# Kernel optimization log

Hardware: AMD Instinct MI355X
Metric: run time of the kernel (lower is better)

## Reference

```python
import jax, jax.numpy as jnp
import numpy as np

B, N, K = 16, 8192, 16
H1, H3 = 512, 64
EPS = 1e-5


def _bn(x, g, b):
    # BatchNorm1d training-mode math: normalize per-channel (last axis) over all other axes.
    ax = tuple(range(x.ndim - 1))
    m = x.mean(ax, keepdims=True)
    v = x.var(ax, keepdims=True)  # biased variance, as in torch BN forward
    return (x - m) * jax.lax.rsqrt(v + EPS) * g + b


def _gather(h, idx):
    # h: [b,n,f], idx: [b,n,k] -> [b,n,k,f] per-batch neighbor gather
    return jax.vmap(lambda hb, ib: hb[ib])(h, idx)


def _forward(data, knn, e1_w, e1_b, e1_g, e1_be,
             gc1_w, gc1_b, g1_g, g1_be, gc2_w, gc2_b, g2_g, g2_be,
             e2_w, e2_b, e2_g, e2_be,
             d1_w, d1_b, d1_g, d1_be, d2_w, d2_b, d2_g, d2_be):
    b, n, _ = data.shape
    # local covariance features
    neigh = _gather(data, knn)                       # [b,n,K,3]
    cen = neigh - neigh.mean(axis=2, keepdims=True)
    cov = jnp.einsum('bnki,bnkj->bnij', cen, cen) / (K - 1)
    x = jnp.concatenate([data, cov.reshape(b, n, 9)], axis=-1)  # [b,n,12]
    # e_layers1: Linear(12,h3) + BN + ReLU
    x = jax.nn.relu(_bn(x @ e1_w + e1_b, e1_g, e1_be))
    # GCNConv over uniform-degree kNN graph with self loop: (h_i + sum_j h_j)/(K+1)
    deg = float(K + 1)
    h = x @ gc1_w
    h = (h + _gather(h, knn).sum(axis=2)) / deg + gc1_b
    x = jax.nn.relu(_bn(h, g1_g, g1_be))
    h = x @ gc2_w
    h = (h + _gather(h, knn).sum(axis=2)) / deg + gc2_b
    x = jax.nn.relu(_bn(h, g2_g, g2_be))             # [b,n,h1]
    # AdaptiveMaxPool1d(1) over nodes
    x = x.max(axis=1, keepdims=True)                 # [b,1,h1]
    # e_layers2: Linear(h1,h1) + BN + ReLU
    x = jax.nn.relu(_bn(x @ e2_w + e2_b, e2_g, e2_be))
    # decode: folding grid
    nx_ = int(1 + (n * 120 / 60) ** 0.5)
    ny_ = int(1 + (n * 60 / 120) ** 0.5)
    xg = jnp.linspace(1.0, 120.0, nx_)
    yg = jnp.linspace(1.0, 60.0, ny_)
    grid = jnp.stack(jnp.meshgrid(xg, yg, indexing='ij'), axis=-1).reshape(-1, 2)[:n]
    kfeat = jnp.broadcast_to(x, (b, n, x.shape[-1]))  # codeword repeated per node
    y = jnp.broadcast_to(grid[None], (b, n, 2))
    z = jnp.concatenate([kfeat, y], axis=-1)          # [b,n,h1+2]
    z = jax.nn.relu(_bn(z @ d1_w + d1_b, d1_g, d1_be))
    z = jnp.concatenate([kfeat, z], axis=-1)          # [b,n,h1+3]
    z = jax.nn.relu(_bn(z @ d2_w + d2_b, d2_g, d2_be))
    return z                                          # [b,n,3]


def setup_inputs() -> dict:
    key = jax.random.key(0)
    ks = jax.random.split(key, 8)

    def lin(k, i, o):
        s = 1.0 / np.sqrt(i)
        return jax.random.uniform(k, (i, o), jnp.float32, -s, s)

    ones = lambda c: jnp.ones((c,), jnp.float32)
    zeros = lambda c: jnp.zeros((c,), jnp.float32)
    return {
        'data': jax.random.normal(ks[0], (B, N, 3), jnp.float32),
        'knn': jax.random.randint(ks[1], (B, N, K), 0, N),
        'e1_w': lin(ks[2], 12, H3), 'e1_b': zeros(H3), 'e1_g': ones(H3), 'e1_be': zeros(H3),
        'gc1_w': lin(ks[3], H3, 2 * H3), 'gc1_b': zeros(2 * H3), 'g1_g': ones(2 * H3), 'g1_be': zeros(2 * H3),
        'gc2_w': lin(ks[4], 2 * H3, H1), 'gc2_b': zeros(H1), 'g2_g': ones(H1), 'g2_be': zeros(H1),
        'e2_w': lin(ks[5], H1, H1), 'e2_b': zeros(H1), 'e2_g': ones(H1), 'e2_be': zeros(H1),
        'd1_w': lin(ks[6], H1 + 2, 3), 'd1_b': zeros(3), 'd1_g': ones(3), 'd1_be': zeros(3),
        'd2_w': lin(ks[7], H1 + 3, 3), 'd2_b': zeros(3), 'd2_g': ones(3), 'd2_be': zeros(3),
    }


def reference(data, knn, e1_w, e1_b, e1_g, e1_be,
              gc1_w, gc1_b, g1_g, g1_be, gc2_w, gc2_b, g2_g, g2_be,
              e2_w, e2_b, e2_g, e2_be,
              d1_w, d1_b, d1_g, d1_be, d2_w, d2_b, d2_g, d2_be):
    return _forward(data, knn, e1_w, e1_b, e1_g, e1_be,
                    gc1_w, gc1_b, g1_g, g1_be, gc2_w, gc2_b, g2_g, g2_be,
                    e2_w, e2_b, e2_g, e2_be,
                    d1_w, d1_b, d1_g, d1_be, d2_w, d2_b, d2_g, d2_be)
```

## Files before the change

kernel.cpp:

```cpp
#include <hip/hip_runtime.h>
#include <hip/hip_fp16.h>
#include <stdint.h>

#define BATCH 16
#define NPTS  8192
#define KNN   16
#define NROWS (BATCH*NPTS)
#define EPSBN 1e-5f
#define DEGINV (1.0f/17.0f)

typedef _Float16 f16x8 __attribute__((ext_vector_type(8)));
typedef float    f32x4 __attribute__((ext_vector_type(4)));

__device__ __forceinline__ unsigned short f2hu(float f) {
    union { _Float16 h; unsigned short u; } cv;
    cv.h = (_Float16)f;
    return cv.u;
}
__device__ __forceinline__ float hu2f(unsigned short u) {
    union { unsigned short u; _Float16 h; } cv;
    cv.u = u;
    return (float)cv.h;
}
__device__ __forceinline__ unsigned fenc(float f) {
    unsigned u = __float_as_uint(f);
    return (int)u >= 0 ? (u | 0x80000000u) : ~u;
}
__device__ __forceinline__ float fdec(unsigned k) {
    return (k & 0x80000000u) ? __uint_as_float(k & 0x7FFFFFFFu) : __uint_as_float(~k);
}

#define SZ_S1    0
#define SZ_S2P   128
#define SZ_S3P   16512
#define SZ_S4    82048
#define SZ_C1    83072
#define SZ_GN    83080
#define SZ_D2    83088
#define SZ_SCSH1 83096
#define SZ_SCSH2 83224
#define SZ_TOT   83480

__global__ __launch_bounds__(256) void k_prep(
    const float* __restrict__ gc1w, const float* __restrict__ gc2w,
    const float* __restrict__ d1w, const float* __restrict__ d1b,
    unsigned short* __restrict__ W1T, unsigned short* __restrict__ W2T,
    float* __restrict__ gn, float* __restrict__ statszone, unsigned* __restrict__ mm)
{
    int t = blockIdx.x * 256 + threadIdx.x;
    int NT_ = gridDim.x * 256;
    for (int i = t; i < 65536; i += NT_) {
        int c = i >> 7, k = i & 127;
        W2T[i] = f2hu(gc2w[k * 512 + c]);
    }
    for (int i = t; i < 8192; i += NT_) {
        int c = i >> 6, k = i & 63;
        W1T[i] = f2hu(gc1w[k * 128 + c]);
    }
    for (int i = t; i < SZ_TOT; i += NT_) statszone[i] = 0.f;
    for (int i = t; i < 8192; i += NT_) mm[i] = 0u;
    for (int i = t; i < 8192; i += NT_) mm[8192 + i] = 0xFFFFFFFFu;
    for (int n = t; n < 8192; n += NT_) {
        int ix = n / 65, iy = n % 65;
        float gx = 1.f + ix * (119.f / 128.f);
        float gy = 1.f + iy * (59.f / 64.f);
        #pragma unroll
        for (int j = 0; j < 3; j++)
            gn[n * 3 + j] = gx * d1w[512 * 3 + j] + gy * d1w[513 * 3 + j] + d1b[j];
    }
}

__global__ __launch_bounds__(256) void k_cov_e1(
    const float* __restrict__ data, const int* __restrict__ knn,
    const float* __restrict__ e1w, const float* __restrict__ e1b,
    float* __restrict__ a1)
{
    __shared__ float w[12 * 64];
    __shared__ float bias[64];
    int tid = threadIdx.x;
    for (int i = tid; i < 768; i += 256) w[i] = e1w[i];
    if (tid < 64) bias[tid] = e1b[tid];
    __syncthreads();

    int gid = blockIdx.x * 256 + tid;
    int b = gid >> 13;
    const float* db = data + (size_t)b * NPTS * 3;
    const int4* k4 = (const int4*)knn + gid * 4;

    float sx = 0, sy = 0, sz = 0, Sxx = 0, Sxy = 0, Sxz = 0, Syy = 0, Syz = 0, Szz = 0;
    #pragma unroll
    for (int jj = 0; jj < 4; jj++) {
        int4 q = k4[jj];
        int id[4] = {q.x, q.y, q.z, q.w};
        #pragma unroll
        for (int u = 0; u < 4; u++) {
            const float* p = db + (size_t)id[u] * 3;
            float x = p[0], y = p[1], z = p[2];
            sx += x; sy += y; sz += z;
            Sxx += x * x; Sxy += x * y; Sxz += x * z;
            Syy += y * y; Syz += y * z; Szz += z * z;
        }
    }
    float mx = sx * (1.f / 16.f), my = sy * (1.f / 16.f), mz = sz * (1.f / 16.f);
    const float inv15 = 1.f / 15.f;
    float x12[12];
    x12[0] = data[(size_t)gid * 3 + 0];
    x12[1] = data[(size_t)gid * 3 + 1];
    x12[2] = data[(size_t)gid * 3 + 2];
    x12[3] = (Sxx - 16.f * mx * mx) * inv15;
    x12[4] = (Sxy - 16.f * mx * my) * inv15;
    x12[5] = (Sxz - 16.f * mx * mz) * inv15;
    x12[6] = x12[4];
    x12[7] = (Syy - 16.f * my * my) * inv15;
    x12[8] = (Syz - 16.f * my * mz) * inv15;
    x12[9] = x12[5];
    x12[10] = x12[8];
    x12[11] = (Szz - 16.f * mz * mz) * inv15;

    float* arow = a1 + (size_t)gid * 64;
    for (int c0 = 0; c0 < 64; c0 += 4) {
        float4 v;
        float* vv = (float*)&v;
        #pragma unroll
        for (int u = 0; u < 4; u++) {
            int c = c0 + u;
            float acc = bias[c];
            #pragma unroll
            for (int i = 0; i < 12; i++) acc += x12[i] * w[i * 64 + c];
            vv[u] = acc;
        }
        *(float4*)(arow + c0) = v;
    }
}

__global__ __launch_bounds__(256) void k_reduce_a1(
    const float* __restrict__ a1, float* __restrict__ stats1)
{
    int tid = threadIdx.x;
    int c = tid & 63, rq = tid >> 6;
    float s = 0.f, q = 0.f;
    for (int row = blockIdx.x * 4 + rq; row < NROWS; row += gridDim.x * 4) {
        float v = a1[(size_t)row * 64 + c];
        s += v; q += v * v;
    }
    __shared__ float red[2][256];
    red[0][tid] = s; red[1][tid] = q;
    __syncthreads();
    if (tid < 64) {
        s = red[0][tid] + red[0][tid + 64] + red[0][tid + 128] + red[0][tid + 192];
        q = red[1][tid] + red[1][tid + 64] + red[1][tid + 128] + red[1][tid + 192];
        atomicAdd(stats1 + tid, s);
        atomicAdd(stats1 + 64 + tid, q);
    }
}

template <int C, int NPARTS>
__global__ __launch_bounds__(256) void k_bncoef(
    const float* __restrict__ statsIn,
    const float* __restrict__ gamma, const float* __restrict__ beta,
    float* __restrict__ scsh)
{
    int ch = threadIdx.x;
    if (ch < C) {
        float s = 0.f, q = 0.f;
        for (int p = 0; p < NPARTS; p++) {
            s += statsIn[p * 2 * C + ch];
            q += statsIn[p * 2 * C + C + ch];
        }
        float m = s * (1.f / NROWS);
        float var = fmaxf(q * (1.f / NROWS) - m * m, 0.f);
        float sc = gamma[ch] * rsqrtf(var + EPSBN);
        scsh[ch] = sc;
        scsh[C + ch] = beta[ch] - m * sc;
    }
}

template <int CIN>
__global__ __launch_bounds__(256) void k_gather(
    const float* __restrict__ ain, const int* __restrict__ knn,
    const float* __restrict__ scsh, unsigned short* __restrict__ S)
{
    constexpr int GPR = CIN / 4;
    constexpr int R = 256 / GPR;
    constexpr int BPB = NPTS / R;

    __shared__ int nidx[R * KNN];

    int tid = threadIdx.x;
    int blk = blockIdx.x;
    int xcd = blk & 7;
    int idx = blk >> 3;
    int batch = xcd + 8 * (idx / BPB);
    int within = idx % BPB;
    int node0 = batch * NPTS + within * R;

    if (tid < R * KNN / 4) {
        const int4* ksrc = (const int4*)(knn + (size_t)node0 * KNN);
        ((int4*)nidx)[tid] = ksrc[tid];
    }
    __syncthreads();

    int t = tid & (GPR - 1);
    int r = tid / GPR;
    int col4 = t * 4;
    float4 scv = *(const float4*)(scsh + col4);
    float4 shv = *(const float4*)(scsh + CIN + col4);

    int row = node0 + r;
    const float* abase = ain + (size_t)batch * NPTS * CIN;

    float4 v = *(const float4*)(ain + (size_t)row * CIN + col4);
    float a0 = fmaxf(v.x * scv.x + shv.x, 0.f);
    float a1v = fmaxf(v.y * scv.y + shv.y, 0.f);
    float a2v = fmaxf(v.z * scv.z + shv.z, 0.f);
    float a3v = fmaxf(v.w * scv.w + shv.w, 0.f);
    #pragma unroll
    for (int jn = 0; jn < KNN; jn++) {
        int src = nidx[r * KNN + jn];
        float4 wv = *(const float4*)(abase + (size_t)src * CIN + col4);
        a0  += fmaxf(wv.x * scv.x + shv.x, 0.f);
        a1v += fmaxf(wv.y * scv.y + shv.y, 0.f);
        a2v += fmaxf(wv.z * scv.z + shv.z, 0.f);
        a3v += fmaxf(wv.w * scv.w + shv.w, 0.f);
    }
    uint2 o;
    o.x = f2hu(a0)  | ((unsigned)f2hu(a1v) << 16);
    o.y = f2hu(a2v) | ((unsigned)f2hu(a3v) << 16);
    *(uint2*)(S + (size_t)row * CIN + col4) = o;
}

template <int CIN>
__global__ __launch_bounds__(256) void k_gather16(
    const unsigned short* __restrict__ ain, const int* __restrict__ knn,
    const float* __restrict__ scsh, unsigned short* __restrict__ S)
{
    constexpr int GPR = CIN / 8;
    constexpr int R = 256 / GPR;
    constexpr int BPB = NPTS / R;

    __shared__ int nidx[R * KNN];

    int tid = threadIdx.x;
    int blk = blockIdx.x;
    int xcd = blk & 7;
    int idx = blk >> 3;
    int batch = xcd + 8 * (idx / BPB);
    int within = idx % BPB;
    int node0 = batch * NPTS + within * R;

    if (tid < R * KNN / 4) {
        const int4* ksrc = (const int4*)(knn + (size_t)node0 * KNN);
        ((int4*)nidx)[tid] = ksrc[tid];
    }
    __syncthreads();

    int t = tid & (GPR - 1);
    int r = tid / GPR;
    int col8 = t * 8;
    float sc8[8], sh8[8];
    #pragma unroll
    for (int j = 0; j < 8; j++) { sc8[j] = scsh[col8 + j]; sh8[j] = scsh[CIN + col8 + j]; }

    int row = node0 + r;
    const unsigned short* abase = ain + (size_t)batch * NPTS * CIN;

    float acc8[8];
    {
        uint4 v = *(const uint4*)(ain + (size_t)row * CIN + col8);
        unsigned wds[4] = {v.x, v.y, v.z, v.w};
        #pragma unroll
        for (int j = 0; j < 4; j++) {
            acc8[2*j]   = fmaxf(hu2f((unsigned short)(wds[j] & 0xFFFF)) * sc8[2*j]   + sh8[2*j],   0.f);
            acc8[2*j+1] = fmaxf(hu2f((unsigned short)(wds[j] >> 16))    * sc8[2*j+1] + sh8[2*j+1], 0.f);
        }
    }
    #pragma unroll
    for (int jn = 0; jn < KNN; jn++) {
        int src = nidx[r * KNN + jn];
        uint4 v = *(const uint4*)(abase + (size_t)src * CIN + col8);
        unsigned wds[4] = {v.x, v.y, v.z, v.w};
        #pragma unroll
        for (int j = 0; j < 4; j++) {
            acc8[2*j]   += fmaxf(hu2f((unsigned short)(wds[j] & 0xFFFF)) * sc8[2*j]   + sh8[2*j],   0.f);
            acc8[2*j+1] += fmaxf(hu2f((unsigned short)(wds[j] >> 16))    * sc8[2*j+1] + sh8[2*j+1], 0.f);
        }
    }
    uint4 o;
    o.x = f2hu(acc8[0]) | ((unsigned)f2hu(acc8[1]) << 16);
    o.y = f2hu(acc8[2]) | ((unsigned)f2hu(acc8[3]) << 16);
    o.z = f2hu(acc8[4]) | ((unsigned)f2hu(acc8[5]) << 16);
    o.w = f2hu(acc8[6]) | ((unsigned)f2hu(acc8[7]) << 16);
    *(uint4*)(S + (size_t)row * CIN + col8) = o;
}

template <int CIN, int COUT, bool STORE>
__global__ __launch_bounds__(256) void k_gemm(
    const unsigned short* __restrict__ S, const unsigned short* __restrict__ WT,
    const float* __restrict__ bias,
    unsigned short* __restrict__ aout, float* __restrict__ statsOut, unsigned* __restrict__ mm)
{
    constexpr int KC = CIN / 32;
    constexpr int NT = COUT / 64;
    constexpr int NHALF = (NT >= 2) ? 2 : 1;
    constexpr int NTH = NT / NHALF;
    constexpr int MT = 64;
    constexpr int SST = CIN + 8;
    constexpr int BPB = NPTS / MT;

    __shared__ alignas(16) unsigned short sA[MT * SST];

    int tid = threadIdx.x;
    int blk = blockIdx.x;
    int xcd = blk & 7;
    int idx = blk >> 3;
    int batch = xcd + 8 * (idx / BPB);
    int within = idx % BPB;
    int node0 = batch * NPTS + within * MT;
    int pout = batch * 4 + (within >> 5);

    {
        constexpr int TOT = MT * CIN / 8;
        const uint4* src = (const uint4*)(S + (size_t)node0 * CIN);
        #pragma unroll
        for (int i = tid; i < TOT; i += 256) {
            int row = i / (CIN / 8);
            int col8 = (i % (CIN / 8)) * 8;
            *(uint4*)&sA[row * SST + col8] = src[i];
        }
    }
    __syncthreads();

    int lane = tid & 63, wv = tid >> 6;
    int n15 = lane & 15, qd = lane >> 4;
    int c0 = wv * (COUT / 4);

    #pragma unroll
    for (int half = 0; half < NHALF; half++) {
        f16x8 wf[KC][NTH];
        float bz[NTH];
        #pragma unroll
        for (int nth = 0; nth < NTH; nth++) {
            int c = c0 + (half * NTH + nth) * 16 + n15;
            bz[nth] = bias[c];
            #pragma unroll
            for (int kc = 0; kc < KC; kc++)
                wf[kc][nth] = *(const f16x8*)(WT + (size_t)c * CIN + kc * 32 + qd * 8);
        }
        float sacc[NTH], qacc[NTH], mxa[NTH], mna[NTH];
        #pragma unroll
        for (int nth = 0; nth < NTH; nth++) {
            sacc[nth] = 0.f; qacc[nth] = 0.f; mxa[nth] = -3.4e38f; mna[nth] = 3.4e38f;
        }

        #pragma unroll
        for (int mt = 0; mt < MT / 16; mt++) {
            f16x8 af[KC];
            #pragma unroll
            for (int kc = 0; kc < KC; kc++)
                af[kc] = *(const f16x8*)&sA[(mt * 16 + n15) * SST + kc * 32 + qd * 8];

            f32x4 acc[NTH];
            #pragma unroll
            for (int nth = 0; nth < NTH; nth++) acc[nth] = (f32x4)(0.f);
            #pragma unroll
            for (int kc = 0; kc < KC; kc++)
                #pragma unroll
                for (int nth = 0; nth < NTH; nth++)
                    acc[nth] = __builtin_amdgcn_mfma_f32_16x16x32_f16(af[kc], wf[kc][nth], acc[nth], 0, 0, 0);

            #pragma unroll
            for (int nth = 0; nth < NTH; nth++) {
                int c = c0 + (half * NTH + nth) * 16 + n15;
                #pragma unroll
                for (int r = 0; r < 4; r++) {
                    float a = acc[nth][r];
                    sacc[nth] += a;
                    qacc[nth] = fmaf(a, a, qacc[nth]);
                    if (!STORE) {
                        mxa[nth] = fmaxf(mxa[nth], a);
                        mna[nth] = fminf(mna[nth], a);
                    }
                    if (STORE) {
                        float v = a * DEGINV + bz[nth];
                        int node = node0 + mt * 16 + qd * 4 + r;
                        aout[(size_t)node * COUT + c] = f2hu(v);
                    }
                }
            }
        }

        #pragma unroll
        for (int nth = 0; nth < NTH; nth++) {
            int c = c0 + (half * NTH + nth) * 16 + n15;
            float S_ = sacc[nth], Q_ = qacc[nth];
            S_ += __shfl_xor(S_, 16); S_ += __shfl_xor(S_, 32);
            Q_ += __shfl_xor(Q_, 16); Q_ += __shfl_xor(Q_, 32);
            if (!STORE) {
                float mx = mxa[nth], mn = mna[nth];
                mx = fmaxf(mx, __shfl_xor(mx, 16)); mx = fmaxf(mx, __shfl_xor(mx, 32));
                mn = fminf(mn, __shfl_xor(mn, 16)); mn = fminf(mn, __shfl_xor(mn, 32));
                if (lane < 16) {
                    atomicMax(mm + batch * COUT + c, fenc(mx * DEGINV + bz[nth]));
                    atomicMin(mm + BATCH * COUT + batch * COUT + c, fenc(mn * DEGINV + bz[nth]));
                }
            }
            if (lane < 16) {
                float b = bz[nth];
                float s = DEGINV * S_ + (float)MT * b;
                float q = DEGINV * DEGINV * Q_ + 2.f * DEGINV * b * S_ + (float)MT * b * b;
                atomicAdd(statsOut + (size_t)pout * 2 * COUT + c, s);
                atomicAdd(statsOut + (size_t)pout * 2 * COUT + COUT + c, q);
            }
        }
    }
}

__global__ __launch_bounds__(256) void k_e2(
    const float* __restrict__ stats3p, const unsigned* __restrict__ mm,
    const float* __restrict__ g2g, const float* __restrict__ g2be,
    const float* __restrict__ e2w, const float* __restrict__ e2b,
    float* __restrict__ a4, float* __restrict__ stats4)
{
    __shared__ float pooled[512];
    int b = blockIdx.x, tid = threadIdx.x;
    for (int c = tid; c < 512; c += 256) {
        float s = 0.f, qq = 0.f;
        for (int p = 0; p < 64; p++) {
            s += stats3p[p * 1024 + c];
            qq += stats3p[p * 1024 + 512 + c];
        }
        float m = s * (1.f / NROWS);
        float var = fmaxf(qq * (1.f / NROWS) - m * m, 0.f);
        float sc = g2g[c] * rsqrtf(var + EPSBN);
        float sh = g2be[c] - m * sc;
        float amax = fdec(mm[b * 512 + c]);
        float amin = fdec(mm[8192 + b * 512 + c]);
        pooled[c] = fmaxf(fmaxf(sc * amax + sh, 0.f), fmaxf(sc * amin + sh, 0.f));
    }
    __syncthreads();
    int ca = tid, cb = tid + 256;
    float acc1 = e2b[ca], acc2 = e2b[cb];
    for (int f = 0; f < 512; f++) {
        float pv = pooled[f];
        acc1 += pv * e2w[f * 512 + ca];
        acc2 += pv * e2w[f * 512 + cb];
    }
    a4[b * 512 + ca] = acc1; a4[b * 512 + cb] = acc2;
    atomicAdd(stats4 + ca, acc1); atomicAdd(stats4 + 512 + ca, acc1 * acc1);
    atomicAdd(stats4 + cb, acc2); atomicAdd(stats4 + 512 + cb, acc2 * acc2);
}

__global__ __launch_bounds__(256) void k_code(
    const float* __restrict__ a4, const float* __restrict__ stats4,
    const float* __restrict__ e2g, const float* __restrict__ e2be,
    const float* __restrict__ d1w, const float* __restrict__ d2w,
    const float* __restrict__ gn,
    float* __restrict__ c1, float* __restrict__ c2,
    float* __restrict__ c1stats, float* __restrict__ gnstats)
{
    int b = blockIdx.x, tid = threadIdx.x;
    int lane = tid & 63, wv = tid >> 6;
    float p1[3] = {0, 0, 0}, p2[3] = {0, 0, 0};
    for (int c = tid; c < 512; c += 256) {
        float s = stats4[c], qq = stats4[512 + c];
        float m = s * (1.f / 16.f);
        float var = fmaxf(qq * (1.f / 16.f) - m * m, 0.f);
        float sc = e2g[c] * rsqrtf(var + EPSBN);
        float sh = e2be[c] - m * sc;
        float cv = fmaxf(sc * a4[b * 512 + c] + sh, 0.f);
        #pragma unroll
        for (int j = 0; j < 3; j++) {
            p1[j] += cv * d1w[c * 3 + j];
            p2[j] += cv * d2w[c * 3 + j];
        }
    }
    __shared__ float red[4][6];
    #pragma unroll
    for (int j = 0; j < 3; j++)
        for (int off = 32; off; off >>= 1) {
            p1[j] += __shfl_xor(p1[j], off);
            p2[j] += __shfl_xor(p2[j], off);
        }
    if (lane == 0) {
        #pragma unroll
        for (int j = 0; j < 3; j++) { red[wv][j] = p1[j]; red[wv][3 + j] = p2[j]; }
    }
    __syncthreads();
    if (tid < 3) {
        float v = red[0][tid] + red[1][tid] + red[2][tid] + red[3][tid];
        c1[b * 3 + tid] = v;
        atomicAdd(c1stats + tid, v);
        atomicAdd(c1stats + 3 + tid, v * v);
    } else if (tid < 6) {
        int j = tid - 3;
        float v = red[0][tid] + red[1][tid] + red[2][tid] + red[3][tid];
        c2[b * 3 + j] = v;
    }
    if (blockIdx.x == 0) {
        float g1[3] = {0, 0, 0}, g2s[3] = {0, 0, 0};
        for (int n = tid; n < NPTS; n += 256) {
            #pragma unroll
            for (int j = 0; j < 3; j++) {
                float g = gn[n * 3 + j];
                g1[j] += g; g2s[j] += g * g;
            }
        }
        #pragma unroll
        for (int j = 0; j < 3; j++)
            for (int off = 32; off; off >>= 1) {
                g1[j] += __shfl_xor(g1[j], off);
                g2s[j] += __shfl_xor(g2s[j], off);
            }
        __shared__ float redg[4][6];
        if (lane == 0) {
            #pragma unroll
            for (int j = 0; j < 3; j++) { redg[wv][j] = g1[j]; redg[wv][3 + j] = g2s[j]; }
        }
        __syncthreads();
        if (tid < 6)
            gnstats[tid] = redg[0][tid] + redg[1][tid] + redg[2][tid] + redg[3][tid];
    }
}

__device__ __forceinline__ void d1_coefs(
    const float* c1stats, const float* gnstats,
    const float* d1g, const float* d1be, float* scd, float* shd)
{
    #pragma unroll
    for (int j = 0; j < 3; j++) {
        float mc = c1stats[j] * (1.f / 16.f), qc = c1stats[3 + j] * (1.f / 16.f);
        float mg = gnstats[j] * (1.f / 8192.f), qg = gnstats[3 + j] * (1.f / 8192.f);
        float m = mc + mg;
        float var = fmaxf((qc - mc * mc) + (qg - mg * mg), 0.f);
        float sc = d1g[j] * rsqrtf(var + EPSBN);
        scd[j] = sc;
        shd[j] = d1be[j] - m * sc;
    }
}

__global__ __launch_bounds__(256) void k_d2stats(
    const float* __restrict__ c1, const float* __restrict__ c2, const float* __restrict__ gn,
    const float* __restrict__ c1stats, const float* __restrict__ gnstats,
    const float* __restrict__ d1g, const float* __restrict__ d1be,
    const float* __restrict__ d2w, const float* __restrict__ d2b,
    float* __restrict__ statsd2)
{
    int gid = blockIdx.x * 256 + threadIdx.x;
    int b = gid >> 13, n = gid & 8191;
    int lane = threadIdx.x & 63, wv = threadIdx.x >> 6;
    float scd[3], shd[3];
    d1_coefs(c1stats, gnstats, d1g, d1be, scd, shd);
    float z3[3];
    #pragma unroll
    for (int j = 0; j < 3; j++)
        z3[j] = fmaxf(scd[j] * (c1[b * 3 + j] + gn[n * 3 + j]) + shd[j], 0.f);
    float vals[6];
    #pragma unroll
    for (int u = 0; u < 3; u++) {
        float a = c2[b * 3 + u]
                + z3[0] * d2w[512 * 3 + u]
                + z3[1] * d2w[513 * 3 + u]
                + z3[2] * d2w[514 * 3 + u]
                + d2b[u];
        vals[u] = a; vals[3 + u] = a * a;
    }
    #pragma unroll
    for (int j = 0; j < 6; j++)
        for (int off = 32; off; off >>= 1) vals[j] += __shfl_xor(vals[j], off);
    __shared__ float red[4][6];
    if (lane == 0) {
        #pragma unroll
        for (int j = 0; j < 6; j++) red[wv][j] = vals[j];
    }
    __syncthreads();
    if (threadIdx.x < 6)
        atomicAdd(statsd2 + threadIdx.x,
                  red[0][threadIdx.x] + red[1][threadIdx.x] + red[2][threadIdx.x] + red[3][threadIdx.x]);
}

__global__ __launch_bounds__(256) void k_out(
    const float* __restrict__ c1, const float* __restrict__ c2, const float* __restrict__ gn,
    const float* __restrict__ c1stats, const float* __restrict__ gnstats,
    const float* __restrict__ statsd2,
    const float* __restrict__ d1g, const float* __restrict__ d1be,
    const float* __restrict__ d2w, const float* __restrict__ d2b,
    const float* __restrict__ d2g, const float* __restrict__ d2be,
    float* __restrict__ out)
{
    int gid = blockIdx.x * 256 + threadIdx.x;
    int b = gid >> 13, n = gid & 8191;
    float scd[3], shd[3];
    d1_coefs(c1stats, gnstats, d1g, d1be, scd, shd);
    float z3[3];
    #pragma unroll
    for (int j = 0; j < 3; j++)
        z3[j] = fmaxf(scd[j] * (c1[b * 3 + j] + gn[n * 3 + j]) + shd[j], 0.f);
    #pragma unroll
    for (int u = 0; u < 3; u++) {
        float a = c2[b * 3 + u]
                + z3[0] * d2w[512 * 3 + u]
                + z3[1] * d2w[513 * 3 + u]
                + z3[2] * d2w[514 * 3 + u]
                + d2b[u];
        float m2 = statsd2[u] * (1.f / (float)NROWS);
        float v2 = fmaxf(statsd2[3 + u] * (1.f / (float)NROWS) - m2 * m2, 0.f);
        float sc = d2g[u] * rsqrtf(v2 + EPSBN);
        float sh = d2be[u] - m2 * sc;
        out[(size_t)gid * 3 + u] = fmaxf(sc * a + sh, 0.f);
    }
}

extern "C" void kernel_launch(void* const* d_in, const int* in_sizes, int n_in,
                              void* d_out, int out_size, void* d_ws, size_t ws_size,
                              hipStream_t stream)
{
    (void)in_sizes; (void)n_in; (void)out_size; (void)ws_size;
    const float* data = (const float*)d_in[0];
    const int*   knn  = (const int*)d_in[1];
    const float* e1w = (const float*)d_in[2],  *e1b = (const float*)d_in[3];
    const float* e1g = (const float*)d_in[4],  *e1be = (const float*)d_in[5];
    const float* gc1w = (const float*)d_in[6], *gc1b = (const float*)d_in[7];
    const float* g1g = (const float*)d_in[8],  *g1be = (const float*)d_in[9];
    const float* gc2w = (const float*)d_in[10], *gc2b = (const float*)d_in[11];
    const float* g2g = (const float*)d_in[12], *g2be = (const float*)d_in[13];
    const float* e2w = (const float*)d_in[14], *e2b = (const float*)d_in[15];
    const float* e2g = (const float*)d_in[16], *e2be = (const float*)d_in[17];
    const float* d1w = (const float*)d_in[18], *d1b = (const float*)d_in[19];
    const float* d1g = (const float*)d_in[20], *d1be = (const float*)d_in[21];
    const float* d2w = (const float*)d_in[22], *d2b = (const float*)d_in[23];
    const float* d2g = (const float*)d_in[24], *d2be = (const float*)d_in[25];

    char* p = (char*)d_ws;
    auto alloc = [&](size_t bytes) -> void* {
        void* r = (void*)p;
        p += (bytes + 255) & ~(size_t)255;
        return r;
    };
    float* a1 = (float*)alloc((size_t)NROWS * 64 * 4);
    unsigned short* a2h = (unsigned short*)alloc((size_t)NROWS * 128 * 2);
    unsigned short* s1 = (unsigned short*)alloc((size_t)NROWS * 64 * 2);
    unsigned short* W1T = (unsigned short*)alloc(8192 * 2);
    unsigned short* W2T = (unsigned short*)alloc(65536 * 2);
    float* statszone = (float*)alloc(SZ_TOT * 4);
    float* stats1  = statszone + SZ_S1;
    float* stats2p = statszone + SZ_S2P;
    float* stats3p = statszone + SZ_S3P;
    float* stats4  = statszone + SZ_S4;
    float* c1stats = statszone + SZ_C1;
    float* gnstats = statszone + SZ_GN;
    float* statsd2 = statszone + SZ_D2;
    float* scsh1   = statszone + SZ_SCSH1;
    float* scsh2   = statszone + SZ_SCSH2;
    unsigned* mm = (unsigned*)alloc(16384 * 4);
    float* a4 = (float*)alloc(16 * 512 * 4);
    float* c1 = (float*)alloc(64 * 4);
    float* c2 = (float*)alloc(64 * 4);
    float* gn = (float*)alloc(8192 * 3 * 4);
    unsigned short* s2 = (unsigned short*)a1;

    k_prep<<<64, 256, 0, stream>>>(gc1w, gc2w, d1w, d1b, W1T, W2T, gn, statszone, mm);
    k_cov_e1<<<512, 256, 0, stream>>>(data, knn, e1w, e1b, a1);
    k_reduce_a1<<<256, 256, 0, stream>>>(a1, stats1);
    k_bncoef<64, 1><<<1, 256, 0, stream>>>(stats1, e1g, e1be, scsh1);
    k_gather<64><<<NROWS / 16, 256, 0, stream>>>(a1, knn, scsh1, s1);
    k_gemm<64, 128, true><<<2048, 256, 0, stream>>>(s1, W1T, gc1b, a2h, stats2p, nullptr);
    k_bncoef<128, 64><<<1, 256, 0, stream>>>(stats2p, g1g, g1be, scsh2);
    k_gather16<128><<<NROWS / 16, 256, 0, stream>>>(a2h, knn, scsh2, s2);
    k_gemm<128, 512, false><<<2048, 256, 0, stream>>>(s2, W2T, gc2b, nullptr, stats3p, mm);
    k_e2<<<16, 256, 0, stream>>>(stats3p, mm, g2g, g2be, e2w, e2b, a4, stats4);
    k_code<<<16, 256, 0, stream>>>(a4, stats4, e2g, e2be, d1w, d2w, gn, c1, c2, c1stats, gnstats);
    k_d2stats<<<512, 256, 0, stream>>>(c1, c2, gn, c1stats, gnstats, d1g, d1be, d2w, d2b, statsd2);
    k_out<<<512, 256, 0, stream>>>(c1, c2, gn, c1stats, gnstats, statsd2,
                                   d1g, d1be, d2w, d2b, d2g, d2be, (float*)d_out);
}
```

Before: 383.2 us.

## Store first-layer activations in fp16 and retile GEMMs with output-column split

The e1 output a1 is now written as fp16 instead of fp32. That halves its write traffic and the read traffic of the reduction and gather passes, and the fp32 gather kernel is dropped in favour of the fp16 gather. The GEMM kernel now uses 128-row tiles and gains an NSPLIT template parameter, so the second GEMM splits its 512 output columns across 4 blocks per tile, and the per-wave weight fragments no longer loop over halves. s2 gets its own buffer instead of aliasing a1. The fp16 rounding of pre-BN activations adds precision risk, and the column split re-stages the A tile into shared memory once per split.

```diff
diff --git a/kernel.cpp b/kernel.cpp
--- a/kernel.cpp
+++ b/kernel.cpp
@@ -73,7 +73,7 @@
 __global__ __launch_bounds__(256) void k_cov_e1(
     const float* __restrict__ data, const int* __restrict__ knn,
     const float* __restrict__ e1w, const float* __restrict__ e1b,
-    float* __restrict__ a1)
+    unsigned short* __restrict__ a1)
 {
     __shared__ float w[12 * 64];
     __shared__ float bias[64];
@@ -117,30 +117,34 @@
     x12[10] = x12[8];
     x12[11] = (Szz - 16.f * mz * mz) * inv15;
 
-    float* arow = a1 + (size_t)gid * 64;
-    for (int c0 = 0; c0 < 64; c0 += 4) {
-        float4 v;
-        float* vv = (float*)&v;
-        #pragma unroll
-        for (int u = 0; u < 4; u++) {
+    unsigned short* arow = a1 + (size_t)gid * 64;
+    for (int c0 = 0; c0 < 64; c0 += 8) {
+        float v8[8];
+        #pragma unroll
+        for (int u = 0; u < 8; u++) {
             int c = c0 + u;
             float acc = bias[c];
             #pragma unroll
             for (int i = 0; i < 12; i++) acc += x12[i] * w[i * 64 + c];
-            vv[u] = acc;
-        }
-        *(float4*)(arow + c0) = v;
+            v8[u] = acc;
+        }
+        uint4 o;
+        o.x = f2hu(v8[0]) | ((unsigned)f2hu(v8[1]) << 16);
+        o.y = f2hu(v8[2]) | ((unsigned)f2hu(v8[3]) << 16);
+        o.z = f2hu(v8[4]) | ((unsigned)f2hu(v8[5]) << 16);
+        o.w = f2hu(v8[6]) | ((unsigned)f2hu(v8[7]) << 16);
+        *(uint4*)(arow + c0) = o;
     }
 }
 
 __global__ __launch_bounds__(256) void k_reduce_a1(
-    const float* __restrict__ a1, float* __restrict__ stats1)
+    const unsigned short* __restrict__ a1, float* __restrict__ stats1)
 {
     int tid = threadIdx.x;
     int c = tid & 63, rq = tid >> 6;
     float s = 0.f, q = 0.f;
     for (int row = blockIdx.x * 4 + rq; row < NROWS; row += gridDim.x * 4) {
-        float v = a1[(size_t)row * 64 + c];
+        float v = hu2f(a1[(size_t)row * 64 + c]);
         s += v; q += v * v;
     }
     __shared__ float red[2][256];
@@ -176,11 +180,11 @@
 }
 
 template <int CIN>
-__global__ __launch_bounds__(256) void k_gather(
-    const float* __restrict__ ain, const int* __restrict__ knn,
+__global__ __launch_bounds__(256) void k_gather16(
+    const unsigned short* __restrict__ ain, const int* __restrict__ knn,
     const float* __restrict__ scsh, unsigned short* __restrict__ S)
 {
-    constexpr int GPR = CIN / 4;
+    constexpr int GPR = CIN / 8;
     constexpr int R = 256 / GPR;
     constexpr int BPB = NPTS / R;
 
@@ -202,60 +206,6 @@
 
     int t = tid & (GPR - 1);
     int r = tid / GPR;
-    int col4 = t * 4;
-    float4 scv = *(const float4*)(scsh + col4);
-    float4 shv = *(const float4*)(scsh + CIN + col4);
-
-    int row = node0 + r;
-    const float* abase = ain + (size_t)batch * NPTS * CIN;
-
-    float4 v = *(const float4*)(ain + (size_t)row * CIN + col4);
-    float a0 = fmaxf(v.x * scv.x + shv.x, 0.f);
-    float a1v = fmaxf(v.y * scv.y + shv.y, 0.f);
-    float a2v = fmaxf(v.z * scv.z + shv.z, 0.f);
-    float a3v = fmaxf(v.w * scv.w + shv.w, 0.f);
-    #pragma unroll
-    for (int jn = 0; jn < KNN; jn++) {
-        int src = nidx[r * KNN + jn];
-        float4 wv = *(const float4*)(abase + (size_t)src * CIN + col4);
-        a0  += fmaxf(wv.x * scv.x + shv.x, 0.f);
-        a1v += fmaxf(wv.y * scv.y + shv.y, 0.f);
-        a2v += fmaxf(wv.z * scv.z + shv.z, 0.f);
-        a3v += fmaxf(wv.w * scv.w + shv.w, 0.f);
-    }
-    uint2 o;
-    o.x = f2hu(a0)  | ((unsigned)f2hu(a1v) << 16);
-    o.y = f2hu(a2v) | ((unsigned)f2hu(a3v) << 16);
-    *(uint2*)(S + (size_t)row * CIN + col4) = o;
-}
-
-template <int CIN>
-__global__ __launch_bounds__(256) void k_gather16(
-    const unsigned short* __restrict__ ain, const int* __restrict__ knn,
-    const float* __restrict__ scsh, unsigned short* __restrict__ S)
-{
-    constexpr int GPR = CIN / 8;
-    constexpr int R = 256 / GPR;
-    constexpr int BPB = NPTS / R;
-
-    __shared__ int nidx[R * KNN];
-
-    int tid = threadIdx.x;
-    int blk = blockIdx.x;
-    int xcd = blk & 7;
-    int idx = blk >> 3;
-    int batch = xcd + 8 * (idx / BPB);
-    int within = idx % BPB;
-    int node0 = batch * NPTS + within * R;
-
-    if (tid < R * KNN / 4) {
-        const int4* ksrc = (const int4*)(knn + (size_t)node0 * KNN);
-        ((int4*)nidx)[tid] = ksrc[tid];
-    }
-    __syncthreads();
-
-    int t = tid & (GPR - 1);
-    int r = tid / GPR;
     int col8 = t * 8;
     float sc8[8], sh8[8];
     #pragma unroll
@@ -293,30 +243,33 @@
     *(uint4*)(S + (size_t)row * CIN + col8) = o;
 }
 
-template <int CIN, int COUT, bool STORE>
+template <int CIN, int COUT, int NSPLIT, bool STORE>
 __global__ __launch_bounds__(256) void k_gemm(
     const unsigned short* __restrict__ S, const unsigned short* __restrict__ WT,
     const float* __restrict__ bias,
     unsigned short* __restrict__ aout, float* __restrict__ statsOut, unsigned* __restrict__ mm)
 {
     constexpr int KC = CIN / 32;
-    constexpr int NT = COUT / 64;
-    constexpr int NHALF = (NT >= 2) ? 2 : 1;
-    constexpr int NTH = NT / NHALF;
-    constexpr int MT = 64;
+    constexpr int MT = 128;
     constexpr int SST = CIN + 8;
-    constexpr int BPB = NPTS / MT;
+    constexpr int CPB = COUT / NSPLIT;
+    constexpr int CPW = CPB / 4;
+    constexpr int NT = CPW / 16;
 
     __shared__ alignas(16) unsigned short sA[MT * SST];
 
     int tid = threadIdx.x;
     int blk = blockIdx.x;
     int xcd = blk & 7;
-    int idx = blk >> 3;
-    int batch = xcd + 8 * (idx / BPB);
-    int within = idx % BPB;
+    int rest = blk >> 3;
+    int nq = rest % NSPLIT;
+    int mseq = rest / NSPLIT;
+    int phase = mseq >> 6;
+    int within = mseq & 63;
+    int batch = xcd + 8 * phase;
     int node0 = batch * NPTS + within * MT;
-    int pout = batch * 4 + (within >> 5);
+    int cbase = nq * CPB;
+    int pout = batch * 4 + (within >> 4);
 
     {
         constexpr int TOT = MT * CIN / 8;
@@ -332,85 +285,82 @@
 
     int lane = tid & 63, wv = tid >> 6;
     int n15 = lane & 15, qd = lane >> 4;
-    int c0 = wv * (COUT / 4);
-
-    #pragma unroll
-    for (int half = 0; half < NHALF; half++) {
-        f16x8 wf[KC][NTH];
-        float bz[NTH];
-        #pragma unroll
-        for (int nth = 0; nth < NTH; nth++) {
-            int c = c0 + (half * NTH + nth) * 16 + n15;
-            bz[nth] = bias[c];
+    int c0 = cbase + wv * CPW;
+
+    f16x8 wf[KC][NT];
+    float bz[NT];
+    #pragma unroll
+    for (int nt = 0; nt < NT; nt++) {
+        int c = c0 + nt * 16 + n15;
+        bz[nt] = bias[c];
+        #pragma unroll
+        for (int kc = 0; kc < KC; kc++)
+            wf[kc][nt] = *(const f16x8*)(WT + (size_t)c * CIN + kc * 32 + qd * 8);
+    }
+    float sacc[NT], qacc[NT], mxa[NT], mna[NT];
+    #pragma unroll
+    for (int nt = 0; nt < NT; nt++) {
+        sacc[nt] = 0.f; qacc[nt] = 0.f; mxa[nt] = -3.4e38f; mna[nt] = 3.4e38f;
+    }
+
+    #pragma unroll
+    for (int mt = 0; mt < MT / 16; mt++) {
+        f16x8 af[KC];
+        #pragma unroll
+        for (int kc = 0; kc < KC; kc++)
+            af[kc] = *(const f16x8*)&sA[(mt * 16 + n15) * SST + kc * 32 + qd * 8];
+
+        f32x4 acc[NT];
+        #pragma unroll
+        for (int nt = 0; nt < NT; nt++) acc[nt] = (f32x4)(0.f);
+        #pragma unroll
+        for (int kc = 0; kc < KC; kc++)
             #pragma unroll
-            for (int kc = 0; kc < KC; kc++)
-                wf[kc][nth] = *(const f16x8*)(WT + (size_t)c * CIN + kc * 32 + qd * 8);
-        }
-        float sacc[NTH], qacc[NTH], mxa[NTH], mna[NTH];
-        #pragma unroll
-        for (int nth = 0; nth < NTH; nth++) {
-            sacc[nth] = 0.f; qacc[nth] = 0.f; mxa[nth] = -3.4e38f; mna[nth] = 3.4e38f;
-        }
-
-        #pragma unroll
-        for (int mt = 0; mt < MT / 16; mt++) {
-            f16x8 af[KC];
+            for (int nt = 0; nt < NT; nt++)
+                acc[nt] = __builtin_amdgcn_mfma_f32_16x16x32_f16(af[kc], wf[kc][nt], acc[nt], 0, 0, 0);
+
+        #pragma unroll
+        for (int nt = 0; nt < NT; nt++) {
+            int c = c0 + nt * 16 + n15;
             #pragma unroll
-            for (int kc = 0; kc < KC; kc++)
-                af[kc] = *(const f16x8*)&sA[(mt * 16 + n15) * SST + kc * 32 + qd * 8];
-
-            f32x4 acc[NTH];
-            #pragma unroll
-            for (int nth = 0; nth < NTH; nth++) acc[nth] = (f32x4)(0.f);
-            #pragma unroll
-            for (int kc = 0; kc < KC; kc++)
-                #pragma unroll
-                for (int nth = 0; nth < NTH; nth++)
-                    acc[nth] = __builtin_amdgcn_mfma_f32_16x16x32_f16(af[kc], wf[kc][nth], acc[nth], 0, 0, 0);
-
-            #pragma unroll
-            for (int nth = 0; nth < NTH; nth++) {
-                int c = c0 + (half * NTH + nth) * 16 + n15;
-                #pragma unroll
-                for (int r = 0; r < 4; r++) {
-                    float a = acc[nth][r];
-                    sacc[nth] += a;
-                    qacc[nth] = fmaf(a, a, qacc[nth]);
-                    if (!STORE) {
-                        mxa[nth] = fmaxf(mxa[nth], a);
-                        mna[nth] = fminf(mna[nth], a);
-                    }
-                    if (STORE) {
-                        float v = a * DEGINV + bz[nth];
-                        int node = node0 + mt * 16 + qd * 4 + r;
-                        aout[(size_t)node * COUT + c] = f2hu(v);
-                    }
+            for (int r = 0; r < 4; r++) {
+                float a = acc[nt][r];
+                sacc[nt] += a;
+                qacc[nt] = fmaf(a, a, qacc[nt]);
+                if (!STORE) {
+                    mxa[nt] = fmaxf(mxa[nt], a);
+                    mna[nt] = fminf(mna[nt], a);
+                }
+                if (STORE) {
+                    float v = a * DEGINV + bz[nt];
+                    int node = node0 + mt * 16 + qd * 4 + r;
+                    aout[(size_t)node * COUT + c] = f2hu(v);
                 }
             }
         }
-
-        #pragma unroll
-        for (int nth = 0; nth < NTH; nth++) {
-            int c = c0 + (half * NTH + nth) * 16 + n15;
-            float S_ = sacc[nth], Q_ = qacc[nth];
-            S_ += __shfl_xor(S_, 16); S_ += __shfl_xor(S_, 32);
-            Q_ += __shfl_xor(Q_, 16); Q_ += __shfl_xor(Q_, 32);
-            if (!STORE) {
-                float mx = mxa[nth], mn = mna[nth];
-                mx = fmaxf(mx, __shfl_xor(mx, 16)); mx = fmaxf(mx, __shfl_xor(mx, 32));
-                mn = fminf(mn, __shfl_xor(mn, 16)); mn = fminf(mn, __shfl_xor(mn, 32));
-                if (lane < 16) {
-                    atomicMax(mm + batch * COUT + c, fenc(mx * DEGINV + bz[nth]));
-                    atomicMin(mm + BATCH * COUT + batch * COUT + c, fenc(mn * DEGINV + bz[nth]));
-                }
+    }
+
+    #pragma unroll
+    for (int nt = 0; nt < NT; nt++) {
+        int c = c0 + nt * 16 + n15;
+        float S_ = sacc[nt], Q_ = qacc[nt];
+        S_ += __shfl_xor(S_, 16); S_ += __shfl_xor(S_, 32);
+        Q_ += __shfl_xor(Q_, 16); Q_ += __shfl_xor(Q_, 32);
+        if (!STORE) {
+            float mx = mxa[nt], mn = mna[nt];
+            mx = fmaxf(mx, __shfl_xor(mx, 16)); mx = fmaxf(mx, __shfl_xor(mx, 32));
+            mn = fminf(mn, __shfl_xor(mn, 16)); mn = fminf(mn, __shfl_xor(mn, 32));
+            if (lane < 16) {
+                atomicMax(mm + batch * COUT + c, fenc(mx * DEGINV + bz[nt]));
+                atomicMin(mm + BATCH * COUT + batch * COUT + c, fenc(mn * DEGINV + bz[nt]));
             }
-            if (lane < 16) {
-                float b = bz[nth];
-                float s = DEGINV * S_ + (float)MT * b;
-                float q = DEGINV * DEGINV * Q_ + 2.f * DEGINV * b * S_ + (float)MT * b * b;
-                atomicAdd(statsOut + (size_t)pout * 2 * COUT + c, s);
-                atomicAdd(statsOut + (size_t)pout * 2 * COUT + COUT + c, q);
-            }
+        }
+        if (lane < 16) {
+            float b = bz[nt];
+            float s = DEGINV * S_ + (float)MT * b;
+            float q = DEGINV * DEGINV * Q_ + 2.f * DEGINV * b * S_ + (float)MT * b * b;
+            atomicAdd(statsOut + (size_t)pout * 2 * COUT + c, s);
+            atomicAdd(statsOut + (size_t)pout * 2 * COUT + COUT + c, q);
         }
     }
 }
@@ -636,9 +586,10 @@
         p += (bytes + 255) & ~(size_t)255;
         return r;
     };
-    float* a1 = (float*)alloc((size_t)NROWS * 64 * 4);
+    unsigned short* a1  = (unsigned short*)alloc((size_t)NROWS * 64 * 2);
     unsigned short* a2h = (unsigned short*)alloc((size_t)NROWS * 128 * 2);
-    unsigned short* s1 = (unsigned short*)alloc((size_t)NROWS * 64 * 2);
+    unsigned short* s1  = (unsigned short*)alloc((size_t)NROWS * 64 * 2);
+    unsigned short* s2  = (unsigned short*)alloc((size_t)NROWS * 128 * 2);
     unsigned short* W1T = (unsigned short*)alloc(8192 * 2);
     unsigned short* W2T = (unsigned short*)alloc(65536 * 2);
     float* statszone = (float*)alloc(SZ_TOT * 4);
@@ -656,17 +607,16 @@
     float* c1 = (float*)alloc(64 * 4);
     float* c2 = (float*)alloc(64 * 4);
     float* gn = (float*)alloc(8192 * 3 * 4);
-    unsigned short* s2 = (unsigned short*)a1;
 
     k_prep<<<64, 256, 0, stream>>>(gc1w, gc2w, d1w, d1b, W1T, W2T, gn, statszone, mm);
     k_cov_e1<<<512, 256, 0, stream>>>(data, knn, e1w, e1b, a1);
     k_reduce_a1<<<256, 256, 0, stream>>>(a1, stats1);
     k_bncoef<64, 1><<<1, 256, 0, stream>>>(stats1, e1g, e1be, scsh1);
-    k_gather<64><<<NROWS / 16, 256, 0, stream>>>(a1, knn, scsh1, s1);
-    k_gemm<64, 128, true><<<2048, 256, 0, stream>>>(s1, W1T, gc1b, a2h, stats2p, nullptr);
+    k_gather16<64><<<NROWS / 32, 256, 0, stream>>>(a1, knn, scsh1, s1);
+    k_gemm<64, 128, 1, true><<<1024, 256, 0, stream>>>(s1, W1T, gc1b, a2h, stats2p, nullptr);
     k_bncoef<128, 64><<<1, 256, 0, stream>>>(stats2p, g1g, g1be, scsh2);
     k_gather16<128><<<NROWS / 16, 256, 0, stream>>>(a2h, knn, scsh2, s2);
-    k_gemm<128, 512, false><<<2048, 256, 0, stream>>>(s2, W2T, gc2b, nullptr, stats3p, mm);
+    k_gemm<128, 512, 4, false><<<4096, 256, 0, stream>>>(s2, W2T, gc2b, nullptr, stats3p, mm);
     k_e2<<<16, 256, 0, stream>>>(stats3p, mm, g2g, g2be, e2w, e2b, a4, stats4);
     k_code<<<16, 256, 0, stream>>>(a4, stats4, e2g, e2be, d1w, d2w, gn, c1, c2, c1stats, gnstats);
     k_d2stats<<<512, 256, 0, stream>>>(c1, c2, gn, c1stats, gnstats, d1g, d1be, d2w, d2b, statsd2);
```

Measured after the change: 334.9 us. 12.6% less time.
